# Kernel optimization log

Hardware: AMD Instinct MI355X
Metric: run time of the kernel (lower is better)

Reference implementation:

```python
import jax, jax.numpy as jnp
import numpy as np

HIDDEN = 4096
NUM_HEADS = 32
HEAD_DIM = HIDDEN // NUM_HEADS
BATCH = 2
SEQ = 2048


def setup_inputs() -> dict:
    key = jax.random.key(0)
    k0, k1, k2, k3 = jax.random.split(key, 4)
    hidden_states = jax.random.normal(k0, (BATCH, SEQ, HIDDEN), dtype=jnp.float32)
    scale = 1.0 / np.sqrt(HIDDEN)
    # torch nn.Linear weight shape: [out_features, in_features]
    wq = jax.random.normal(k1, (HIDDEN, HIDDEN), dtype=jnp.float32) * scale
    wk = jax.random.normal(k2, (HIDDEN, HIDDEN), dtype=jnp.float32) * scale
    wv = jax.random.normal(k3, (HIDDEN, HIDDEN), dtype=jnp.float32) * scale
    return {"hidden_states": hidden_states, "wq": wq, "wk": wk, "wv": wv}


def reference(hidden_states, wq, wk, wv):
    b, s, _ = hidden_states.shape
    # torch Linear: y = x @ W.T
    q = hidden_states @ wq.T
    k = hidden_states @ wk.T
    v = hidden_states @ wv.T
    # [b, s, h, d] -> [b, h, s, d]
    q = q.reshape(b, s, NUM_HEADS, HEAD_DIM).transpose(0, 2, 1, 3)
    k = k.reshape(b, s, NUM_HEADS, HEAD_DIM).transpose(0, 2, 1, 3)
    v = v.reshape(b, s, NUM_HEADS, HEAD_DIM).transpose(0, 2, 1, 3)
    attn_weights = jnp.einsum('bhqd,bhkd->bhqk', q, k) / np.sqrt(HEAD_DIM)
    attn_weights = jax.nn.softmax(attn_weights, axis=-1)
    out = jnp.einsum('bhqk,bhkd->bhqd', attn_weights, v)
    out = out.transpose(0, 2, 1, 3).reshape(b, s, HIDDEN)
    return (out, attn_weights)
```

## Files before the change

### kernel.cpp

```cpp
#include <hip/hip_runtime.h>

typedef __attribute__((ext_vector_type(8))) short short8v;
typedef __attribute__((ext_vector_type(4))) float f32x4;
typedef __attribute__((ext_vector_type(16))) float f32x16;

#define HID 4096
#define SEQL 2048
#define NH 32
#define HD 128
#define MROWS 4096


__device__ __forceinline__ void gl_lds16(const void* g, void* l) {
  __builtin_amdgcn_global_load_lds(
      (const __attribute__((address_space(1))) unsigned int*)g,
      (__attribute__((address_space(3))) unsigned int*)l, 16, 0, 0);
}

__device__ __forceinline__ unsigned short f2bf(float x) {
  union { float f; unsigned u; } v; v.f = x;
  return (unsigned short)((v.u + 0x7FFFu + ((v.u >> 16) & 1u)) >> 16);
}


__global__ __launch_bounds__(256) void cast_bf16_kernel(
    const float* __restrict__ s0, const float* __restrict__ s1,
    const float* __restrict__ s2, const float* __restrict__ s3,
    unsigned short* __restrict__ dst)
{
  const float* src = blockIdx.y == 0 ? s0 : blockIdx.y == 1 ? s1
                   : blockIdx.y == 2 ? s2 : s3;
  unsigned short* d = dst + (size_t)blockIdx.y * ((size_t)HID * MROWS);
  size_t i = (size_t)blockIdx.x * blockDim.x + threadIdx.x;
  const float4* s4 = (const float4*)src;
  float4 a = s4[2 * i], b = s4[2 * i + 1];
  short8v o;
  o[0] = (short)f2bf(a.x); o[1] = (short)f2bf(a.y);
  o[2] = (short)f2bf(a.z); o[3] = (short)f2bf(a.w);
  o[4] = (short)f2bf(b.x); o[5] = (short)f2bf(b.y);
  o[6] = (short)f2bf(b.z); o[7] = (short)f2bf(b.w);
  *(short8v*)(d + i * 8) = o;
}

__global__ __launch_bounds__(256) void gemm_qkv_kernel(
    const unsigned short* __restrict__ A,
    const unsigned short* __restrict__ Wq,
    const unsigned short* __restrict__ Wk,
    const unsigned short* __restrict__ Wv,
    unsigned short* __restrict__ Qo,
    unsigned short* __restrict__ Ko,
    unsigned short* __restrict__ Vo)
{
  __shared__ unsigned short As[128 * 64];
  __shared__ unsigned short Bs[128 * 64];
  const int which = blockIdx.x >> 10;
  const int id = blockIdx.x & 1023;
  const unsigned short* W = which == 0 ? Wq : which == 1 ? Wk : Wv;
  unsigned short* C = which == 0 ? Qo : which == 1 ? Ko : Vo;

  const int t = threadIdx.x;
  const int lane = t & 63;
  const int w = t >> 6;
  const int wr = w >> 1, wc = w & 1;
  const int bm = (id >> 5) << 7;
  const int bn = (id & 31) << 7;

  f32x4 acc[4][4] = {};

  const int srow = t >> 3;
  const int sslot = t & 7;

  for (int k0 = 0; k0 < HID; k0 += 64) {
#pragma unroll
    for (int i = 0; i < 4; ++i) {
      int row = i * 32 + srow;
      int cola = k0 + ((sslot ^ (row & 7)) << 3);
      gl_lds16(&A[(size_t)(bm + row) * HID + cola], (char*)As + i * 4096 + w * 1024);
      gl_lds16(&W[(size_t)(bn + row) * HID + cola], (char*)Bs + i * 4096 + w * 1024);
    }
    __syncthreads();
#pragma unroll
    for (int c = 0; c < 2; ++c) {
      short8v av[4], bv[4];
#pragma unroll
      for (int m = 0; m < 4; ++m) {
        int row = wr * 64 + m * 16 + (lane & 15);
        int phys = (c * 4 + (lane >> 4)) ^ (row & 7);
        av[m] = *(const short8v*)&As[row * 64 + phys * 8];
      }
#pragma unroll
      for (int n = 0; n < 4; ++n) {
        int row = wc * 64 + n * 16 + (lane & 15);
        int phys = (c * 4 + (lane >> 4)) ^ (row & 7);
        bv[n] = *(const short8v*)&Bs[row * 64 + phys * 8];
      }
#pragma unroll
      for (int m = 0; m < 4; ++m)
#pragma unroll
        for (int n = 0; n < 4; ++n)
          acc[m][n] = __builtin_amdgcn_mfma_f32_16x16x32_bf16(av[m], bv[n], acc[m][n], 0, 0, 0);
    }
    __syncthreads();
  }

#pragma unroll
  for (int m = 0; m < 4; ++m) {
#pragma unroll
    for (int n = 0; n < 4; ++n) {
      int r0 = bm + wr * 64 + m * 16 + (lane >> 4) * 4;
      int col = bn + wc * 64 + n * 16 + (lane & 15);
      if (which < 2) {
#pragma unroll
        for (int j = 0; j < 4; ++j)
          C[(size_t)(r0 + j) * HID + col] = f2bf(acc[m][n][j]);
      } else {
        int head = col >> 7, dd = col & 127;
        int bb = r0 >> 11, s = r0 & 2047;
        unsigned short* p = C + ((size_t)(bb * NH + head) * HD + dd) * (size_t)SEQL + s;
        union { unsigned short us[4]; uint2 v; } pk;
        pk.us[0] = f2bf(acc[m][n][0]); pk.us[1] = f2bf(acc[m][n][1]);
        pk.us[2] = f2bf(acc[m][n][2]); pk.us[3] = f2bf(acc[m][n][3]);
        *(uint2*)p = pk.v;
      }
    }
  }
}

__global__ __launch_bounds__(256) void attn_kernel(
    const unsigned short* __restrict__ Q,
    const unsigned short* __restrict__ K,
    const unsigned short* __restrict__ Vt,
    float* __restrict__ attn_out,
    float* __restrict__ out)
{
  const int flat = blockIdx.x;
  const int sw = (flat & 7) * 128 + (flat >> 3);
  const int q0 = (sw & 15) << 7;
  const int bh = sw >> 4;
  const int b = bh >> 5, h = bh & 31;
  const int t = threadIdx.x, lane = t & 63, w = t >> 6;
  const int l31 = lane & 31, g = lane >> 5;
  const float a = 0.08838834764831845f * 1.4426950408889634f;

  __shared__ unsigned short Ks[2 * 64 * 128];
  __shared__ unsigned short Vs[2 * 128 * 64];
  __shared__ unsigned short Ps[4][32 * 64];

  short8v qf[8];
  {
    const unsigned short* qrow =
        Q + (size_t)(b * SEQL + q0 + w * 32 + l31) * HID + h * HD + g * 8;
#pragma unroll
    for (int c = 0; c < 8; ++c) qf[c] = *(const short8v*)(qrow + c * 16);
  }

  const int krow_s = t >> 4;
  const int kchunk_s = t & 15;
  const int vrow_s = t >> 3;
  const int vchunk_s = t & 7;

  float lsum[16];
#pragma unroll
  for (int r = 0; r < 16; ++r) lsum[r] = 0.f;

  {
#pragma unroll
    for (int i = 0; i < 4; ++i) {
      int krow = i * 16 + krow_s;
      int kchunk = kchunk_s ^ (krow & 15);
      gl_lds16(&K[(size_t)(b * SEQL + krow) * HID + h * HD + kchunk * 8],
               (char*)Ks + i * 4096 + w * 1024);
    }
  }
  __syncthreads();
  int buf = 0;
  for (int kt = 0; kt < SEQL; kt += 64) {
    if (kt + 64 < SEQL) {
#pragma unroll
      for (int i = 0; i < 4; ++i) {
        int krow = i * 16 + krow_s;
        int kchunk = kchunk_s ^ (krow & 15);
        gl_lds16(&K[(size_t)(b * SEQL + kt + 64 + krow) * HID + h * HD + kchunk * 8],
                 (char*)Ks + (buf ^ 1) * 16384 + i * 4096 + w * 1024);
      }
    }
    const unsigned short* Kc = Ks + buf * 8192;
    f32x16 s0 = {}, s1 = {};
    __builtin_amdgcn_s_setprio(1);
#pragma unroll
    for (int c = 0; c < 8; ++c) {
      int r0 = l31;
      short8v k0v = *(const short8v*)&Kc[r0 * 128 + (((c * 2 + g) ^ (r0 & 15)) * 8)];
      int r1 = 32 + l31;
      short8v k1v = *(const short8v*)&Kc[r1 * 128 + (((c * 2 + g) ^ (r1 & 15)) * 8)];
      s0 = __builtin_amdgcn_mfma_f32_32x32x16_bf16(qf[c], k0v, s0, 0, 0, 0);
      s1 = __builtin_amdgcn_mfma_f32_32x32x16_bf16(qf[c], k1v, s1, 0, 0, 0);
    }
    __builtin_amdgcn_s_setprio(0);
#pragma unroll
    for (int r = 0; r < 16; ++r)
      lsum[r] += exp2f(s0[r] * a) + exp2f(s1[r] * a);
    __syncthreads();
    buf ^= 1;
  }

  float lb[16];
#pragma unroll
  for (int r = 0; r < 16; ++r) {
    float e = lsum[r];
#pragma unroll
    for (int d = 1; d < 32; d <<= 1) e += __shfl_xor(e, d);
    lb[r] = -__log2f(e);
  }

  f32x16 o[4] = {};
  float* abase = attn_out + ((size_t)bh * SEQL + q0 + w * 32) * (size_t)SEQL + l31;

  {
#pragma unroll
    for (int i = 0; i < 4; ++i) {
      int krow = i * 16 + krow_s;
      int kchunk = kchunk_s ^ (krow & 15);
      gl_lds16(&K[(size_t)(b * SEQL + krow) * HID + h * HD + kchunk * 8],
               (char*)Ks + i * 4096 + w * 1024);
      int vrow = i * 32 + vrow_s;
      int vchunk = vchunk_s ^ (vrow & 7);
      gl_lds16(&Vt[((size_t)bh * HD + vrow) * (size_t)SEQL + vchunk * 8],
               (char*)Vs + i * 4096 + w * 1024);
    }
  }
  __syncthreads();
  buf = 0;
  for (int kt = 0; kt < SEQL; kt += 64) {
    if (kt + 64 < SEQL) {
#pragma unroll
      for (int i = 0; i < 4; ++i) {
        int krow = i * 16 + krow_s;
        int kchunk = kchunk_s ^ (krow & 15);
        gl_lds16(&K[(size_t)(b * SEQL + kt + 64 + krow) * HID + h * HD + kchunk * 8],
                 (char*)Ks + (buf ^ 1) * 16384 + i * 4096 + w * 1024);
        int vrow = i * 32 + vrow_s;
        int vchunk = vchunk_s ^ (vrow & 7);
        gl_lds16(&Vt[((size_t)bh * HD + vrow) * (size_t)SEQL + kt + 64 + vchunk * 8],
                 (char*)Vs + (buf ^ 1) * 16384 + i * 4096 + w * 1024);
      }
    }
    const unsigned short* Kc = Ks + buf * 8192;
    const unsigned short* Vc = Vs + buf * 8192;
    f32x16 s0 = {}, s1 = {};
    __builtin_amdgcn_s_setprio(1);
#pragma unroll
    for (int c = 0; c < 8; ++c) {
      int r0 = l31;
      short8v k0v = *(const short8v*)&Kc[r0 * 128 + (((c * 2 + g) ^ (r0 & 15)) * 8)];
      int r1 = 32 + l31;
      short8v k1v = *(const short8v*)&Kc[r1 * 128 + (((c * 2 + g) ^ (r1 & 15)) * 8)];
      s0 = __builtin_amdgcn_mfma_f32_32x32x16_bf16(qf[c], k0v, s0, 0, 0, 0);
      s1 = __builtin_amdgcn_mfma_f32_32x32x16_bf16(qf[c], k1v, s1, 0, 0, 0);
    }
    __builtin_amdgcn_s_setprio(0);
#pragma unroll
    for (int r = 0; r < 16; ++r) {
      int qr = (r & 3) + ((r >> 2) << 3) + g * 4;
      float p0 = exp2f(__builtin_fmaf(s0[r], a, lb[r]));
      float p1 = exp2f(__builtin_fmaf(s1[r], a, lb[r]));
      __builtin_nontemporal_store(p0, &abase[(size_t)qr * SEQL + kt]);
      __builtin_nontemporal_store(p1, &abase[(size_t)qr * SEQL + kt + 32]);
      int sl0 = ((l31 >> 3)) ^ (qr & 7);
      int sl1 = (4 + (l31 >> 3)) ^ (qr & 7);
      Ps[w][qr * 64 + sl0 * 8 + (l31 & 7)] = f2bf(p0);
      Ps[w][qr * 64 + sl1 * 8 + (l31 & 7)] = f2bf(p1);
    }
    __builtin_amdgcn_s_setprio(1);
#pragma unroll
    for (int c2 = 0; c2 < 4; ++c2) {
      short8v pa = *(const short8v*)&Ps[w][l31 * 64 + (((c2 * 2 + g) ^ (l31 & 7)) * 8)];
#pragma unroll
      for (int n = 0; n < 4; ++n) {
        int vrow = n * 32 + l31;
        short8v vb = *(const short8v*)&Vc[vrow * 64 + (((c2 * 2 + g) ^ (vrow & 7)) * 8)];
        o[n] = __builtin_amdgcn_mfma_f32_32x32x16_bf16(pa, vb, o[n], 0, 0, 0);
      }
    }
    __builtin_amdgcn_s_setprio(0);
    __syncthreads();
    buf ^= 1;
  }

  float* obase = out + (size_t)(b * SEQL + q0 + w * 32) * HID + h * HD + l31;
#pragma unroll
  for (int n = 0; n < 4; ++n)
#pragma unroll
    for (int r = 0; r < 16; ++r) {
      int qr = (r & 3) + ((r >> 2) << 3) + g * 4;
      __builtin_nontemporal_store(o[n][r], &obase[(size_t)qr * HID + n * 32]);
    }
}


extern "C" void kernel_launch(void* const* d_in, const int* in_sizes, int n_in,
                              void* d_out, int out_size, void* d_ws, size_t ws_size,
                              hipStream_t stream) {
  const float* X  = (const float*)d_in[0];
  const float* wq = (const float*)d_in[1];
  const float* wk = (const float*)d_in[2];
  const float* wv = (const float*)d_in[3];

  const size_t NEL = (size_t)HID * MROWS;
  unsigned short* ws  = (unsigned short*)d_ws;
  unsigned short* Xb  = ws;
  unsigned short* Wqb = ws + NEL;
  unsigned short* Wkb = ws + 2 * NEL;
  unsigned short* Wvb = ws + 3 * NEL;
  unsigned short* Qb  = ws + 4 * NEL;
  unsigned short* Kb  = ws + 5 * NEL;
  unsigned short* Vtb = ws + 6 * NEL;

  float* outp  = (float*)d_out;
  float* attnp = outp + NEL;

  cast_bf16_kernel<<<dim3(8192, 4), 256, 0, stream>>>(X, wq, wk, wv, Xb);
  gemm_qkv_kernel<<<3072, 256, 0, stream>>>(Xb, Wqb, Wkb, Wvb, Qb, Kb, Vtb);
  attn_kernel<<<1024, 256, 0, stream>>>(Qb, Kb, Vtb, attnp, outp);
}
```

Measured before the change: 866.1 us.

## Restructure QKV GEMM into 256x256 tiles with a double-buffered, barrier-interleaved pipeline

```diff
diff --git a/kernel.cpp b/kernel.cpp
--- a/kernel.cpp
+++ b/kernel.cpp
@@ -21,6 +21,11 @@
   union { float f; unsigned u; } v; v.f = x;
   return (unsigned short)((v.u + 0x7FFFu + ((v.u >> 16) & 1u)) >> 16);
 }
+
+#define BAR()    __builtin_amdgcn_s_barrier()
+#define LGKM0()  asm volatile("s_waitcnt lgkmcnt(0)" ::: "memory")
+#define VM4()    asm volatile("s_waitcnt vmcnt(4)" ::: "memory")
+#define SCHED0() __builtin_amdgcn_sched_barrier(0)
 
 
 __global__ __launch_bounds__(256) void cast_bf16_kernel(
@@ -42,7 +47,7 @@
   *(short8v*)(d + i * 8) = o;
 }
 
-__global__ __launch_bounds__(256) void gemm_qkv_kernel(
+__global__ __launch_bounds__(512, 2) void gemm_qkv_kernel(
     const unsigned short* __restrict__ A,
     const unsigned short* __restrict__ Wq,
     const unsigned short* __restrict__ Wk,
@@ -51,63 +56,89 @@
     unsigned short* __restrict__ Ko,
     unsigned short* __restrict__ Vo)
 {
-  __shared__ unsigned short As[128 * 64];
-  __shared__ unsigned short Bs[128 * 64];
-  const int which = blockIdx.x >> 10;
-  const int id = blockIdx.x & 1023;
+  __shared__ unsigned short As[2 * 256 * 64];
+  __shared__ unsigned short Bs[2 * 256 * 64];
+  const int which = blockIdx.x >> 8;
+  const int id = blockIdx.x & 255;
   const unsigned short* W = which == 0 ? Wq : which == 1 ? Wk : Wv;
   unsigned short* C = which == 0 ? Qo : which == 1 ? Ko : Vo;
 
   const int t = threadIdx.x;
   const int lane = t & 63;
   const int w = t >> 6;
-  const int wr = w >> 1, wc = w & 1;
-  const int bm = (id >> 5) << 7;
-  const int bn = (id & 31) << 7;
-
-  f32x4 acc[4][4] = {};
+  const int wr = w >> 2, wc = w & 3;
+  const int bm = (id >> 4) << 8;
+  const int bn = (id & 15) << 8;
 
   const int srow = t >> 3;
   const int sslot = t & 7;
-
-  for (int k0 = 0; k0 < HID; k0 += 64) {
-#pragma unroll
-    for (int i = 0; i < 4; ++i) {
-      int row = i * 32 + srow;
-      int cola = k0 + ((sslot ^ (row & 7)) << 3);
-      gl_lds16(&A[(size_t)(bm + row) * HID + cola], (char*)As + i * 4096 + w * 1024);
-      gl_lds16(&W[(size_t)(bn + row) * HID + cola], (char*)Bs + i * 4096 + w * 1024);
-    }
-    __syncthreads();
-#pragma unroll
-    for (int c = 0; c < 2; ++c) {
-      short8v av[4], bv[4];
-#pragma unroll
-      for (int m = 0; m < 4; ++m) {
-        int row = wr * 64 + m * 16 + (lane & 15);
-        int phys = (c * 4 + (lane >> 4)) ^ (row & 7);
-        av[m] = *(const short8v*)&As[row * 64 + phys * 8];
-      }
-#pragma unroll
-      for (int n = 0; n < 4; ++n) {
-        int row = wc * 64 + n * 16 + (lane & 15);
-        int phys = (c * 4 + (lane >> 4)) ^ (row & 7);
-        bv[n] = *(const short8v*)&Bs[row * 64 + phys * 8];
-      }
-#pragma unroll
-      for (int m = 0; m < 4; ++m)
-#pragma unroll
-        for (int n = 0; n < 4; ++n)
-          acc[m][n] = __builtin_amdgcn_mfma_f32_16x16x32_bf16(av[m], bv[n], acc[m][n], 0, 0, 0);
-    }
-    __syncthreads();
-  }
-
-#pragma unroll
-  for (int m = 0; m < 4; ++m) {
+  const int scol = (sslot ^ (srow & 7)) << 3;
+  const size_t arow0 = (size_t)(bm + srow) * HID;
+  const size_t brow0 = (size_t)(bn + srow) * HID;
+  const int ldsoff = (t & ~63) << 4;
+
+#define STAGE(isB, tile, half) do {                                          \
+    int _k = ((tile) & 63) << 6;                                             \
+    const unsigned short* _s = (isB) ? W : A;                                \
+    size_t _r = ((isB) ? brow0 : arow0) + (size_t)(half) * 128 * HID;        \
+    char* _d = (char*)((isB) ? Bs : As) + ((tile) & 1) * 32768 +             \
+               (half) * 16384 + ldsoff;                                      \
+    gl_lds16(&_s[_r + _k + scol], _d);                                       \
+    gl_lds16(&_s[_r + (size_t)64 * HID + _k + scol], _d + 8192);             \
+  } while (0)
+
+  short8v av[4][2];
+  short8v bv[2][4];
+  f32x4 acc[8][4] = {};
+
+#define RD_A(d, mbase)                                                        \
+  _Pragma("unroll") for (int mm = 0; mm < 4; ++mm) {                          \
+    int row = wr * 128 + ((mbase) + mm) * 16 + (lane & 15);                   \
+    av[mm][0] = *(const short8v*)&As[(d)*16384 + row*64 + ((   (lane>>4)) ^ (row&7))*8]; \
+    av[mm][1] = *(const short8v*)&As[(d)*16384 + row*64 + ((4+ (lane>>4)) ^ (row&7))*8]; \
+  }
+#define RD_B(d, kk)                                                           \
+  _Pragma("unroll") for (int nn = 0; nn < 4; ++nn) {                          \
+    int row = wc * 64 + nn * 16 + (lane & 15);                                \
+    bv[kk][nn] = *(const short8v*)&Bs[(d)*16384 + row*64 + (((kk)*4 + (lane>>4)) ^ (row&7))*8]; \
+  }
+#define MFMA16(mbase, kk)                                                     \
+  __builtin_amdgcn_s_setprio(1);                                              \
+  _Pragma("unroll") for (int mm = 0; mm < 4; ++mm)                            \
+  _Pragma("unroll") for (int nn = 0; nn < 4; ++nn)                            \
+    acc[(mbase)+mm][nn] = __builtin_amdgcn_mfma_f32_16x16x32_bf16(            \
+        av[mm][kk], bv[kk][nn], acc[(mbase)+mm][nn], 0, 0, 0);                \
+  __builtin_amdgcn_s_setprio(0);
+
+  STAGE(1, 0, 0); STAGE(1, 0, 1); STAGE(0, 0, 0); STAGE(0, 0, 1);
+  STAGE(1, 1, 0); STAGE(1, 1, 1);
+  VM4(); BAR();
+
+  for (int i = 0; i < 32; ++i) {
+    int j = 2 * i;
+    RD_A(0, 0); RD_B(0, 0); STAGE(0, j + 1, 0);
+    SCHED0(); BAR(); LGKM0(); SCHED0(); MFMA16(0, 0); SCHED0(); BAR();
+    RD_B(0, 1); STAGE(0, j + 1, 1);
+    SCHED0(); BAR(); LGKM0(); SCHED0(); MFMA16(0, 1); SCHED0(); BAR();
+    RD_A(0, 4); STAGE(1, j + 2, 0);
+    SCHED0(); BAR(); LGKM0(); SCHED0(); MFMA16(4, 0); SCHED0(); BAR();
+    STAGE(0, j + 2, 0); VM4();
+    SCHED0(); BAR(); SCHED0(); MFMA16(4, 1); SCHED0(); BAR();
+    RD_A(1, 0); RD_B(1, 0); STAGE(1, j + 2, 1);
+    SCHED0(); BAR(); LGKM0(); SCHED0(); MFMA16(0, 0); SCHED0(); BAR();
+    RD_B(1, 1); STAGE(0, j + 2, 1);
+    SCHED0(); BAR(); LGKM0(); SCHED0(); MFMA16(0, 1); SCHED0(); BAR();
+    RD_A(1, 4); STAGE(1, j + 3, 0);
+    SCHED0(); BAR(); LGKM0(); SCHED0(); MFMA16(4, 0); SCHED0(); BAR();
+    STAGE(1, j + 3, 1); VM4();
+    SCHED0(); BAR(); SCHED0(); MFMA16(4, 1); SCHED0(); BAR();
+  }
+
+#pragma unroll
+  for (int m = 0; m < 8; ++m) {
 #pragma unroll
     for (int n = 0; n < 4; ++n) {
-      int r0 = bm + wr * 64 + m * 16 + (lane >> 4) * 4;
+      int r0 = bm + wr * 128 + m * 16 + (lane >> 4) * 4;
       int col = bn + wc * 64 + n * 16 + (lane & 15);
       if (which < 2) {
 #pragma unroll
@@ -124,6 +155,10 @@
       }
     }
   }
+#undef STAGE
+#undef RD_A
+#undef RD_B
+#undef MFMA16
 }
 
 __global__ __launch_bounds__(256) void attn_kernel(
@@ -320,6 +355,6 @@
   float* attnp = outp + NEL;
 
   cast_bf16_kernel<<<dim3(8192, 4), 256, 0, stream>>>(X, wq, wk, wv, Xb);
-  gemm_qkv_kernel<<<3072, 256, 0, stream>>>(Xb, Wqb, Wkb, Wvb, Qb, Kb, Vtb);
+  gemm_qkv_kernel<<<768, 512, 0, stream>>>(Xb, Wqb, Wkb, Wvb, Qb, Kb, Vtb);
   attn_kernel<<<1024, 256, 0, stream>>>(Qb, Kb, Vtb, attnp, outp);
 }
```

New measurement: 802.1 us. 7.4% less time.
